# Kernel tuning notes

Hardware: AMD Instinct MI355X
Metric: run time of the kernel (lower is better)

Reference implementation:

```python
import jax, jax.numpy as jnp
import numpy as np

N_CLASSES = 80
TOPK = 13
ALPHA = 1.0
BETA = 6.0
EPS = 1e-9
BS, N_ANCHORS, N_MAX = 32, 8400, 100


def setup_inputs() -> dict:
    key = jax.random.key(0)
    k1, k2, k3, k4, k5, k6 = jax.random.split(key, 6)
    pred_scores = jax.random.uniform(k1, (BS, N_ANCHORS, N_CLASSES), dtype=jnp.float32)
    anchor_points = jax.random.uniform(k2, (N_ANCHORS, 2), dtype=jnp.float32) * 640.0
    # predicted boxes centered on anchor points (valid xyxy)
    wh = jax.random.uniform(k3, (BS, N_ANCHORS, 2), dtype=jnp.float32) * 100.0 + 4.0
    ctr = anchor_points[None]
    pred_bboxes = jnp.concatenate([ctr - wh / 2, ctr + wh / 2], axis=-1)
    gt_lt = jax.random.uniform(k4, (BS, N_MAX, 2), dtype=jnp.float32) * 500.0
    gt_wh = jax.random.uniform(k5, (BS, N_MAX, 2), dtype=jnp.float32) * 120.0 + 8.0
    gt_bboxes = jnp.concatenate([gt_lt, gt_lt + gt_wh], axis=-1)
    gt_labels = jax.random.randint(k6, (BS, N_MAX, 1), 0, N_CLASSES).astype(jnp.int32)
    mask_gt = jnp.ones((BS, N_MAX, 1), dtype=jnp.float32)
    return {"pred_scores": pred_scores, "pred_bboxes": pred_bboxes,
            "anchor_points": anchor_points, "gt_labels": gt_labels,
            "gt_bboxes": gt_bboxes, "mask_gt": mask_gt}


def _batch_iou(a, b):
    # a: [bs, n, 4], b: [bs, m, 4] (xyxy) -> [bs, n, m]
    lt = jnp.maximum(a[:, :, None, :2], b[:, None, :, :2])
    rb = jnp.minimum(a[:, :, None, 2:], b[:, None, :, 2:])
    wh = jnp.clip(rb - lt, 0.0)
    inter = wh[..., 0] * wh[..., 1]
    area_a = ((a[..., 2] - a[..., 0]) * (a[..., 3] - a[..., 1]))[:, :, None]
    area_b = ((b[..., 2] - b[..., 0]) * (b[..., 3] - b[..., 1]))[:, None, :]
    return inter / (area_a + area_b - inter + EPS)


def _assign(pred_scores, pred_bboxes, anchor_points, gt_labels, gt_bboxes, mask_gt):
    bs, n_anchors, n_classes = pred_scores.shape
    n_max = gt_bboxes.shape[1]
    labels = gt_labels[..., 0].astype(jnp.int32)  # [bs, n_max]

    # alignment metric: bbox_scores[b,g,a] = pred_scores[b,a,labels[b,g]]
    ps_t = jnp.swapaxes(pred_scores, 1, 2)  # [bs, C, n_anchors]
    bbox_scores = jnp.take_along_axis(ps_t, labels[:, :, None], axis=1)  # [bs, n_max, n_anchors]
    overlaps = _batch_iou(gt_bboxes, pred_bboxes)  # [bs, n_max, n_anchors]
    align_metric = jnp.power(bbox_scores, ALPHA) * jnp.power(overlaps, BETA)

    # anchor centers inside gt boxes
    ap = anchor_points[None, None, :, :]  # [1,1,n_anchors,2]
    deltas = jnp.concatenate(
        [ap - gt_bboxes[:, :, None, :2], gt_bboxes[:, :, None, 2:] - ap], axis=-1)
    is_in_gts = (deltas.min(axis=-1) > EPS).astype(align_metric.dtype)  # [bs,n_max,n_anchors]

    # topk candidate selection
    metrics = align_metric * is_in_gts
    _, topk_idxs = jax.lax.top_k(metrics, TOPK)  # [bs, n_max, TOPK]
    topk_mask = (mask_gt > 0)  # [bs, n_max, 1], broadcasts over TOPK
    topk_idxs = jnp.where(topk_mask, topk_idxs, 0)

    def count_row(idx):  # idx: [TOPK] -> anchor hit counts [n_anchors]
        return jnp.zeros((n_anchors,), jnp.int32).at[idx].add(1)
    counts = jax.vmap(jax.vmap(count_row))(topk_idxs)  # [bs, n_max, n_anchors]
    is_in_topk = jnp.where(counts > 1, 0, counts).astype(metrics.dtype)

    mask_pos = is_in_topk * is_in_gts * mask_gt  # [bs, n_max, n_anchors]

    # fix collisions: anchors assigned to multiple GTs keep the max-IoU GT
    mask_pos_sum = mask_pos.sum(axis=1)  # [bs, n_anchors]
    multi = mask_pos_sum[:, None, :] > 1
    is_max_overlaps = jax.nn.one_hot(overlaps.argmax(axis=1), n_max, axis=1,
                                     dtype=mask_pos.dtype)  # [bs, n_max, n_anchors]
    mask_pos = jnp.where(multi, is_max_overlaps, mask_pos)
    mask_pos_sum = mask_pos.sum(axis=1)
    assigned_gt_idx = mask_pos.argmax(axis=1)  # [bs, n_anchors]

    # final assignments via flattened gather
    flat_idx = assigned_gt_idx + jnp.arange(bs, dtype=jnp.int32)[:, None] * n_max
    assigned_labels = labels.reshape(-1)[flat_idx]  # [bs, n_anchors]
    assigned_bboxes = gt_bboxes.reshape(-1, 4)[flat_idx]  # [bs, n_anchors, 4]
    assigned_labels = jnp.where(assigned_labels < 0, 0, assigned_labels)
    assigned_scores = jax.nn.one_hot(assigned_labels, n_classes, dtype=pred_scores.dtype)
    pos = mask_pos_sum > 0
    assigned_scores = jnp.where(pos[..., None], assigned_scores, 0.0)
    assigned_labels = jnp.where(pos, assigned_labels, n_classes)

    # normalize scores by alignment metric
    align_metric = align_metric * mask_pos
    pos_align = align_metric.max(axis=-1, keepdims=True)  # [bs, n_max, 1]
    pos_overlaps = (overlaps * mask_pos).max(axis=-1, keepdims=True)
    norm = (align_metric * pos_overlaps / (pos_align + EPS)).max(axis=1)[..., None]  # [bs,n_anchors,1]
    assigned_scores = assigned_scores * norm

    return assigned_labels, assigned_bboxes, assigned_scores, pos


def reference(pred_scores, pred_bboxes, anchor_points, gt_labels, gt_bboxes, mask_gt):
    return _assign(pred_scores, pred_bboxes, anchor_points, gt_labels, gt_bboxes, mask_gt)
```

## Files before the change

kernel.cpp:

```cpp
#include <hip/hip_runtime.h>

#define BS 32
#define NA 8400
#define NMAX 100
#define NC 80
#define TOPK 13
#define EPSF 1e-9f
#define WCAP 1024
#define NSTRIP 64
#define STRIP_INV 0.1f

#define OFF_LBL  0
#define OFF_BOX  (BS*NA)
#define OFF_SCR  (BS*NA + BS*NA*4)
#define OFF_POS  (BS*NA + BS*NA*4 + BS*NA*NC)

#define NBA_ELEMS (BS*NA)
#define ZERO_U32  (NBA_ELEMS + 2*BS*NMAX)

__device__ __forceinline__ float iou_fn(float gx1, float gy1, float gx2, float gy2,
                                        float px1, float py1, float px2, float py2) {
    float lx = fmaxf(gx1, px1), ly = fmaxf(gy1, py1);
    float rx = fminf(gx2, px2), ry = fminf(gy2, py2);
    float w = fmaxf(rx - lx, 0.f), h = fmaxf(ry - ly, 0.f);
    float inter = w * h;
    float aa = (gx2 - gx1) * (gy2 - gy1);
    float ab = (px2 - px1) * (py2 - py1);
    return inter / (aa + ab - inter + EPSF);
}

__global__ __launch_bounds__(1024) void bin_zero_kernel(
    const float* __restrict__ anchor_points,
    int* __restrict__ strip_off, float4* __restrict__ sAPI,
    unsigned int* __restrict__ zero_base)
{
    int t = threadIdx.x;
    if (blockIdx.x != 0) {
        uint4* z = (uint4*)zero_base;
        const int nz = ZERO_U32 / 4;
        uint4 zz = make_uint4(0u, 0u, 0u, 0u);
        for (int i = (blockIdx.x - 1) * 1024 + t; i < nz; i += 8 * 1024)
            z[i] = zz;
        return;
    }

    __shared__ int cnt[NSTRIP];
    __shared__ int cur[NSTRIP];
    if (t < NSTRIP) cnt[t] = 0;
    __syncthreads();
    const float2* ap2 = (const float2*)anchor_points;
    for (int a = t; a < NA; a += 1024) {
        int s = (int)(ap2[a].y * STRIP_INV);
        s = s < 0 ? 0 : (s > NSTRIP - 1 ? NSTRIP - 1 : s);
        atomicAdd(&cnt[s], 1);
    }
    __syncthreads();
    if (t < 64) {
        int v = cnt[t];
        int inc = v;
        #pragma unroll
        for (int d = 1; d < 64; d <<= 1) {
            int o = __shfl_up(inc, d, 64);
            if (t >= d) inc += o;
        }
        int excl = inc - v;
        cur[t] = excl; strip_off[t] = excl;
        if (t == 63) strip_off[64] = inc;
    }
    __syncthreads();
    for (int a = t; a < NA; a += 1024) {
        float2 p = ap2[a];
        int s = (int)(p.y * STRIP_INV);
        s = s < 0 ? 0 : (s > NSTRIP - 1 ? NSTRIP - 1 : s);
        int pos = atomicAdd(&cur[s], 1);
        sAPI[pos] = make_float4(p.x, p.y, __int_as_float(a), 0.f);
    }
}

__global__ __launch_bounds__(256) void topk_kernel(
    const float* __restrict__ pred_scores,
    const float* __restrict__ pred_bboxes,
    const int*   __restrict__ gt_labels,
    const float* __restrict__ gt_bboxes,
    const float* __restrict__ mask_gt,
    const int*   __restrict__ strip_off,
    const float4* __restrict__ sAPI,
    unsigned int* __restrict__ claims)
{
    __shared__ unsigned short aidx[4][WCAP];
    int wave = threadIdx.x >> 6;
    int lane = threadIdx.x & 63;
    int row = blockIdx.x * 4 + wave;
    int b = row / NMAX, j = row % NMAX;
    if (mask_gt[row] <= 0.f) return;

    const float* gbp = gt_bboxes + (size_t)row * 4;
    float gx1 = gbp[0], gy1 = gbp[1], gx2 = gbp[2], gy2 = gbp[3];
    int lab = gt_labels[row];

    int s_lo = (int)(gy1 * STRIP_INV); s_lo = s_lo < 0 ? 0 : (s_lo > NSTRIP-1 ? NSTRIP-1 : s_lo);
    int s_hi = (int)(gy2 * STRIP_INV); s_hi = s_hi < 0 ? 0 : (s_hi > NSTRIP-1 ? NSTRIP-1 : s_hi);
    int lo = strip_off[s_lo], hi = strip_off[s_hi + 1];

    int cnt = 0;
    for (int base = lo; base < hi; base += 64) {
        int p = base + lane;
        bool hit = false; int a = 0;
        if (p < hi) {
            float4 ap = sAPI[p];
            a = __float_as_int(ap.z);
            hit = (ap.x - gx1 > EPSF) && (ap.y - gy1 > EPSF) &&
                  (gx2 - ap.x > EPSF) && (gy2 - ap.y > EPSF);
        }
        unsigned long long mb = __ballot(hit);
        if (hit) {
            int my = cnt + __popcll(mb & ((1ULL << lane) - 1ULL));
            if (my < WCAP) aidx[wave][my] = (unsigned short)a;
        }
        cnt += __popcll(mb);
    }
    if (cnt > WCAP) cnt = WCAP;

    unsigned long long loc[TOPK];
    #pragma unroll
    for (int i = 0; i < TOPK; i++) loc[i] = 0ULL;
    const float4* pb4 = (const float4*)pred_bboxes;
    for (int p = lane; p < cnt; p += 64) {
        int a = aidx[wave][p];
        float4 pb = pb4[b * NA + a];
        float s = pred_scores[((size_t)b * NA + a) * NC + lab];
        float iou = iou_fn(gx1, gy1, gx2, gy2, pb.x, pb.y, pb.z, pb.w);
        float i2 = iou * iou;
        float m = s * (i2 * i2 * i2);
        if (m > 0.f) {
            unsigned long long key =
                ((unsigned long long)__float_as_uint(m) << 32) |
                (unsigned int)(NA - a);
            #pragma unroll
            for (int i = 0; i < TOPK; i++) {
                if (key > loc[i]) { unsigned long long tmp = loc[i]; loc[i] = key; key = tmp; }
            }
        }
    }

    for (int r = 0; r < TOPK; r++) {
        unsigned long long h = loc[0];
        unsigned long long m = h;
        #pragma unroll
        for (int s = 32; s > 0; s >>= 1) {
            unsigned long long o = __shfl_xor(m, s, 64);
            m = o > m ? o : m;
        }
        if (m == 0ULL) break;
        unsigned long long ball = __ballot(h == m);
        if (lane == (int)__builtin_ctzll(ball)) {
            #pragma unroll
            for (int i = 0; i < TOPK - 1; i++) loc[i] = loc[i + 1];
            loc[TOPK - 1] = 0ULL;
            int a = NA - (int)(unsigned int)(m & 0xFFFFFFFFULL);
            atomicAdd(&claims[b * NA + a], (1u << 16) | (unsigned int)j);
        }
    }
}

__global__ __launch_bounds__(256) void resolve_kernel(
    const float* __restrict__ pred_scores,
    const float* __restrict__ pred_bboxes,
    const int*   __restrict__ gt_labels,
    const float* __restrict__ gt_bboxes,
    const unsigned int* __restrict__ claims,
    int* __restrict__ assigned_j, float* __restrict__ a_align,
    unsigned int* __restrict__ pa_bits, unsigned int* __restrict__ po_bits)
{
    __shared__ float4 gtb[NMAX];
    __shared__ int    glab[NMAX];
    int b = blockIdx.y;
    int t = threadIdx.x;
    if (t < NMAX) {
        gtb[t]  = ((const float4*)gt_bboxes)[b * NMAX + t];
        glab[t] = gt_labels[b * NMAX + t];
    }
    __syncthreads();

    int ai = blockIdx.x * 256 + t;
    if (ai >= NA) return;
    int idx = b * NA + ai;
    unsigned int pk = claims[idx];
    if (pk == 0u) { assigned_j[idx] = -1; a_align[idx] = 0.f; return; }

    float4 pb = ((const float4*)pred_bboxes)[idx];

    int js; float iou;
    if ((pk >> 16) == 1u) {
        js = (int)(pk & 0xFFFFu);
        float4 g = gtb[js];
        iou = iou_fn(g.x, g.y, g.z, g.w, pb.x, pb.y, pb.z, pb.w);
    } else {
        float best = -1.f; js = 0;
        for (int j = 0; j < NMAX; j++) {
            float4 g = gtb[j];
            float v = iou_fn(g.x, g.y, g.z, g.w, pb.x, pb.y, pb.z, pb.w);
            if (v > best) { best = v; js = j; }
        }
        iou = best;
    }
    int lab = glab[js];
    float s = pred_scores[(size_t)idx * NC + lab];
    float i2 = iou * iou;
    float align = s * (i2 * i2 * i2);
    assigned_j[idx] = js; a_align[idx] = align;
    atomicMax(&pa_bits[b * NMAX + js], __float_as_uint(align));
    atomicMax(&po_bits[b * NMAX + js], __float_as_uint(iou));
}

__global__ __launch_bounds__(256) void finalize_kernel(
    const int*   __restrict__ gt_labels,
    const float* __restrict__ gt_bboxes,
    const int* __restrict__ assigned_j,
    const float* __restrict__ a_align,
    const unsigned int* __restrict__ pa_bits, const unsigned int* __restrict__ po_bits,
    float* __restrict__ out)
{
    int t = threadIdx.x;
    int idx = blockIdx.x * 256 + t;
    int b = idx / NA;
    int js = assigned_j[idx];
    bool pos = js >= 0;
    int j0 = pos ? js : 0;
    int lab = gt_labels[b * NMAX + j0];

    out[OFF_LBL + idx] = pos ? (float)lab : (float)NC;

    float4 gb = ((const float4*)gt_bboxes)[b * NMAX + j0];
    ((float4*)(out + OFF_BOX))[idx] = gb;

    out[OFF_POS + idx] = pos ? 1.f : 0.f;

    float4* sc = (float4*)(out + OFF_SCR + (size_t)blockIdx.x * 256 * NC);
    float4 z = make_float4(0.f, 0.f, 0.f, 0.f);
    #pragma unroll
    for (int i = 0; i < 256 * NC / 4 / 256; i++)
        sc[t + i * 256] = z;
    __syncthreads();

    if (pos) {
        float pa = __uint_as_float(pa_bits[b * NMAX + js]);
        float po = __uint_as_float(po_bits[b * NMAX + js]);
        float norm = a_align[idx] * po / (pa + EPSF);
        out[OFF_SCR + (size_t)idx * NC + lab] = norm;
    }
}

extern "C" void kernel_launch(void* const* d_in, const int* in_sizes, int n_in,
                              void* d_out, int out_size, void* d_ws, size_t ws_size,
                              hipStream_t stream) {
    const float* pred_scores   = (const float*)d_in[0];
    const float* pred_bboxes   = (const float*)d_in[1];
    const float* anchor_points = (const float*)d_in[2];
    const int*   gt_labels     = (const int*)d_in[3];
    const float* gt_bboxes     = (const float*)d_in[4];
    const float* mask_gt       = (const float*)d_in[5];

    char* ws = (char*)d_ws;
    const size_t NBA = (size_t)BS * NA;
    unsigned int* claims   = (unsigned int*)(ws);
    unsigned int* pa_bits  = (unsigned int*)(ws + NBA * 4);
    unsigned int* po_bits  = (unsigned int*)(ws + NBA * 4 + (size_t)BS * NMAX * 4);
    int*   assigned_j = (int*)(ws + NBA * 4 + (size_t)BS * NMAX * 8);
    float* a_align    = (float*)(ws + NBA * 8 + (size_t)BS * NMAX * 8);
    size_t off5 = NBA * 12 + (size_t)BS * NMAX * 8;
    int*    strip_off = (int*)(ws + off5);
    float4* sAPI      = (float4*)(ws + off5 + 512);

    float* out = (float*)d_out;

    bin_zero_kernel<<<9, 1024, 0, stream>>>(anchor_points, strip_off, sAPI, claims);

    topk_kernel<<<BS * NMAX / 4, 256, 0, stream>>>(
        pred_scores, pred_bboxes, gt_labels, gt_bboxes, mask_gt,
        strip_off, sAPI, claims);

    dim3 rgrid((NA + 255) / 256, BS);
    resolve_kernel<<<rgrid, 256, 0, stream>>>(
        pred_scores, pred_bboxes, gt_labels, gt_bboxes, claims,
        assigned_j, a_align, pa_bits, po_bits);

    finalize_kernel<<<(int)(NBA / 256), 256, 0, stream>>>(
        gt_labels, gt_bboxes, assigned_j, a_align, pa_bits, po_bits, out);
}
```

Before: 231.7 us.

## Drop binning kernel, emit per-GT top-k lists, move score zeroing into topk launch

Removes the anchor strip-binning kernel and has each top-k wave scan all anchors directly. Instead of global atomic claims per anchor, each GT row writes its top-k anchor list and count, and the resolve kernel rebuilds per-anchor claims in shared memory from those lists. Zeroing of the large score output and the pa/po buffers moves into extra blocks of the top-k launch, so it can overlap with the top-k work, and is removed from finalize. This cuts one launch and the global claims buffer traffic. In exchange, every wave scans all 8400 anchors instead of a y-strip, and each resolve block rescans all 1300 list entries.

```diff
diff --git a/kernel.cpp b/kernel.cpp
--- a/kernel.cpp
+++ b/kernel.cpp
@@ -7,16 +7,16 @@
 #define TOPK 13
 #define EPSF 1e-9f
 #define WCAP 1024
-#define NSTRIP 64
-#define STRIP_INV 0.1f
 
 #define OFF_LBL  0
 #define OFF_BOX  (BS*NA)
 #define OFF_SCR  (BS*NA + BS*NA*4)
 #define OFF_POS  (BS*NA + BS*NA*4 + BS*NA*NC)
 
-#define NBA_ELEMS (BS*NA)
-#define ZERO_U32  (NBA_ELEMS + 2*BS*NMAX)
+#define NROWS (BS*NMAX)
+#define TKBLK 800
+#define ZBLK  250
+#define NSC4  (BS*NA*NC/4)
 
 __device__ __forceinline__ float iou_fn(float gx1, float gy1, float gx2, float gy2,
                                         float px1, float py1, float px2, float py2) {
@@ -29,93 +29,61 @@
     return inter / (aa + ab - inter + EPSF);
 }
 
-__global__ __launch_bounds__(1024) void bin_zero_kernel(
-    const float* __restrict__ anchor_points,
-    int* __restrict__ strip_off, float4* __restrict__ sAPI,
-    unsigned int* __restrict__ zero_base)
-{
-    int t = threadIdx.x;
-    if (blockIdx.x != 0) {
-        uint4* z = (uint4*)zero_base;
-        const int nz = ZERO_U32 / 4;
-        uint4 zz = make_uint4(0u, 0u, 0u, 0u);
-        for (int i = (blockIdx.x - 1) * 1024 + t; i < nz; i += 8 * 1024)
-            z[i] = zz;
-        return;
-    }
-
-    __shared__ int cnt[NSTRIP];
-    __shared__ int cur[NSTRIP];
-    if (t < NSTRIP) cnt[t] = 0;
-    __syncthreads();
-    const float2* ap2 = (const float2*)anchor_points;
-    for (int a = t; a < NA; a += 1024) {
-        int s = (int)(ap2[a].y * STRIP_INV);
-        s = s < 0 ? 0 : (s > NSTRIP - 1 ? NSTRIP - 1 : s);
-        atomicAdd(&cnt[s], 1);
-    }
-    __syncthreads();
-    if (t < 64) {
-        int v = cnt[t];
-        int inc = v;
-        #pragma unroll
-        for (int d = 1; d < 64; d <<= 1) {
-            int o = __shfl_up(inc, d, 64);
-            if (t >= d) inc += o;
-        }
-        int excl = inc - v;
-        cur[t] = excl; strip_off[t] = excl;
-        if (t == 63) strip_off[64] = inc;
-    }
-    __syncthreads();
-    for (int a = t; a < NA; a += 1024) {
-        float2 p = ap2[a];
-        int s = (int)(p.y * STRIP_INV);
-        s = s < 0 ? 0 : (s > NSTRIP - 1 ? NSTRIP - 1 : s);
-        int pos = atomicAdd(&cur[s], 1);
-        sAPI[pos] = make_float4(p.x, p.y, __int_as_float(a), 0.f);
-    }
-}
-
 __global__ __launch_bounds__(256) void topk_kernel(
     const float* __restrict__ pred_scores,
     const float* __restrict__ pred_bboxes,
+    const float* __restrict__ anchor_points,
     const int*   __restrict__ gt_labels,
     const float* __restrict__ gt_bboxes,
     const float* __restrict__ mask_gt,
-    const int*   __restrict__ strip_off,
-    const float4* __restrict__ sAPI,
-    unsigned int* __restrict__ claims)
+    unsigned int*   __restrict__ ccount,
+    unsigned short* __restrict__ clist,
+    unsigned int* __restrict__ pa_bits,
+    unsigned int* __restrict__ po_bits,
+    float* __restrict__ out)
 {
+    int t = threadIdx.x;
+    if (blockIdx.x >= TKBLK) {
+        int zb = blockIdx.x - TKBLK;
+        if (zb == 0) {
+            uint4* pz = (uint4*)pa_bits;
+            uint4 zz = make_uint4(0u, 0u, 0u, 0u);
+            for (int i = t; i < 1600; i += 256) pz[i] = zz;
+        }
+        float4* sz = (float4*)(out + OFF_SCR);
+        float4 zf = make_float4(0.f, 0.f, 0.f, 0.f);
+        for (int i = zb * 256 + t; i < NSC4; i += ZBLK * 256) sz[i] = zf;
+        return;
+    }
+
     __shared__ unsigned short aidx[4][WCAP];
-    int wave = threadIdx.x >> 6;
-    int lane = threadIdx.x & 63;
+    int wave = t >> 6;
+    int lane = t & 63;
     int row = blockIdx.x * 4 + wave;
-    int b = row / NMAX, j = row % NMAX;
-    if (mask_gt[row] <= 0.f) return;
+    if (mask_gt[row] <= 0.f) {
+        if (lane == 0) ccount[row] = 0u;
+        return;
+    }
+    int b = row / NMAX;
 
     const float* gbp = gt_bboxes + (size_t)row * 4;
     float gx1 = gbp[0], gy1 = gbp[1], gx2 = gbp[2], gy2 = gbp[3];
     int lab = gt_labels[row];
 
-    int s_lo = (int)(gy1 * STRIP_INV); s_lo = s_lo < 0 ? 0 : (s_lo > NSTRIP-1 ? NSTRIP-1 : s_lo);
-    int s_hi = (int)(gy2 * STRIP_INV); s_hi = s_hi < 0 ? 0 : (s_hi > NSTRIP-1 ? NSTRIP-1 : s_hi);
-    int lo = strip_off[s_lo], hi = strip_off[s_hi + 1];
-
+    const float2* ap2 = (const float2*)anchor_points;
     int cnt = 0;
-    for (int base = lo; base < hi; base += 64) {
+    for (int base = 0; base < NA; base += 64) {
         int p = base + lane;
-        bool hit = false; int a = 0;
-        if (p < hi) {
-            float4 ap = sAPI[p];
-            a = __float_as_int(ap.z);
+        bool hit = false;
+        if (p < NA) {
+            float2 ap = ap2[p];
             hit = (ap.x - gx1 > EPSF) && (ap.y - gy1 > EPSF) &&
                   (gx2 - ap.x > EPSF) && (gy2 - ap.y > EPSF);
         }
         unsigned long long mb = __ballot(hit);
         if (hit) {
             int my = cnt + __popcll(mb & ((1ULL << lane) - 1ULL));
-            if (my < WCAP) aidx[wave][my] = (unsigned short)a;
+            if (my < WCAP) aidx[wave][my] = (unsigned short)p;
         }
         cnt += __popcll(mb);
     }
@@ -143,6 +111,7 @@
         }
     }
 
+    int picks = TOPK;
     for (int r = 0; r < TOPK; r++) {
         unsigned long long h = loc[0];
         unsigned long long m = h;
@@ -151,16 +120,17 @@
             unsigned long long o = __shfl_xor(m, s, 64);
             m = o > m ? o : m;
         }
-        if (m == 0ULL) break;
+        if (m == 0ULL) { picks = r; break; }
         unsigned long long ball = __ballot(h == m);
         if (lane == (int)__builtin_ctzll(ball)) {
             #pragma unroll
             for (int i = 0; i < TOPK - 1; i++) loc[i] = loc[i + 1];
             loc[TOPK - 1] = 0ULL;
             int a = NA - (int)(unsigned int)(m & 0xFFFFFFFFULL);
-            atomicAdd(&claims[b * NA + a], (1u << 16) | (unsigned int)j);
-        }
-    }
+            clist[row * TOPK + r] = (unsigned short)a;
+        }
+    }
+    if (lane == 0) ccount[row] = (unsigned int)picks;
 }
 
 __global__ __launch_bounds__(256) void resolve_kernel(
@@ -168,28 +138,43 @@
     const float* __restrict__ pred_bboxes,
     const int*   __restrict__ gt_labels,
     const float* __restrict__ gt_bboxes,
-    const unsigned int* __restrict__ claims,
+    const unsigned int*   __restrict__ ccount,
+    const unsigned short* __restrict__ clist,
     int* __restrict__ assigned_j, float* __restrict__ a_align,
     unsigned int* __restrict__ pa_bits, unsigned int* __restrict__ po_bits)
 {
     __shared__ float4 gtb[NMAX];
     __shared__ int    glab[NMAX];
+    __shared__ int    ccnt[NMAX];
+    __shared__ unsigned int pkl[256];
     int b = blockIdx.y;
     int t = threadIdx.x;
     if (t < NMAX) {
         gtb[t]  = ((const float4*)gt_bboxes)[b * NMAX + t];
         glab[t] = gt_labels[b * NMAX + t];
-    }
+        ccnt[t] = (int)ccount[b * NMAX + t];
+    }
+    pkl[t] = 0u;
     __syncthreads();
 
-    int ai = blockIdx.x * 256 + t;
+    int lo = blockIdx.x * 256;
+    for (int e = t; e < NMAX * TOPK; e += 256) {
+        int j = e / TOPK, k = e - j * TOPK;
+        if (k < ccnt[j]) {
+            int a = clist[(b * NMAX + j) * TOPK + k];
+            unsigned int w = (unsigned int)(a - lo);
+            if (w < 256u) atomicAdd(&pkl[w], (1u << 16) | (unsigned int)j);
+        }
+    }
+    __syncthreads();
+
+    int ai = lo + t;
     if (ai >= NA) return;
     int idx = b * NA + ai;
-    unsigned int pk = claims[idx];
+    unsigned int pk = pkl[t];
     if (pk == 0u) { assigned_j[idx] = -1; a_align[idx] = 0.f; return; }
 
     float4 pb = ((const float4*)pred_bboxes)[idx];
-
     int js; float iou;
     if ((pk >> 16) == 1u) {
         js = (int)(pk & 0xFFFFu);
@@ -230,24 +215,13 @@
     int lab = gt_labels[b * NMAX + j0];
 
     out[OFF_LBL + idx] = pos ? (float)lab : (float)NC;
-
-    float4 gb = ((const float4*)gt_bboxes)[b * NMAX + j0];
-    ((float4*)(out + OFF_BOX))[idx] = gb;
-
+    ((float4*)(out + OFF_BOX))[idx] = ((const float4*)gt_bboxes)[b * NMAX + j0];
     out[OFF_POS + idx] = pos ? 1.f : 0.f;
-
-    float4* sc = (float4*)(out + OFF_SCR + (size_t)blockIdx.x * 256 * NC);
-    float4 z = make_float4(0.f, 0.f, 0.f, 0.f);
-    #pragma unroll
-    for (int i = 0; i < 256 * NC / 4 / 256; i++)
-        sc[t + i * 256] = z;
-    __syncthreads();
 
     if (pos) {
         float pa = __uint_as_float(pa_bits[b * NMAX + js]);
         float po = __uint_as_float(po_bits[b * NMAX + js]);
-        float norm = a_align[idx] * po / (pa + EPSF);
-        out[OFF_SCR + (size_t)idx * NC + lab] = norm;
+        out[OFF_SCR + (size_t)idx * NC + lab] = a_align[idx] * po / (pa + EPSF);
     }
 }
 
@@ -263,26 +237,22 @@
 
     char* ws = (char*)d_ws;
     const size_t NBA = (size_t)BS * NA;
-    unsigned int* claims   = (unsigned int*)(ws);
-    unsigned int* pa_bits  = (unsigned int*)(ws + NBA * 4);
-    unsigned int* po_bits  = (unsigned int*)(ws + NBA * 4 + (size_t)BS * NMAX * 4);
-    int*   assigned_j = (int*)(ws + NBA * 4 + (size_t)BS * NMAX * 8);
-    float* a_align    = (float*)(ws + NBA * 8 + (size_t)BS * NMAX * 8);
-    size_t off5 = NBA * 12 + (size_t)BS * NMAX * 8;
-    int*    strip_off = (int*)(ws + off5);
-    float4* sAPI      = (float4*)(ws + off5 + 512);
+    unsigned int*   pa_bits = (unsigned int*)(ws);
+    unsigned int*   po_bits = (unsigned int*)(ws + 12800);
+    unsigned int*   ccount  = (unsigned int*)(ws + 25600);
+    unsigned short* clist   = (unsigned short*)(ws + 38400);
+    int*   assigned_j = (int*)(ws + 38400 + (size_t)NROWS * TOPK * 2 + 320);
+    float* a_align    = (float*)((char*)assigned_j + NBA * 4);
 
     float* out = (float*)d_out;
 
-    bin_zero_kernel<<<9, 1024, 0, stream>>>(anchor_points, strip_off, sAPI, claims);
-
-    topk_kernel<<<BS * NMAX / 4, 256, 0, stream>>>(
-        pred_scores, pred_bboxes, gt_labels, gt_bboxes, mask_gt,
-        strip_off, sAPI, claims);
+    topk_kernel<<<TKBLK + ZBLK, 256, 0, stream>>>(
+        pred_scores, pred_bboxes, anchor_points, gt_labels, gt_bboxes, mask_gt,
+        ccount, clist, pa_bits, po_bits, out);
 
     dim3 rgrid((NA + 255) / 256, BS);
     resolve_kernel<<<rgrid, 256, 0, stream>>>(
-        pred_scores, pred_bboxes, gt_labels, gt_bboxes, claims,
+        pred_scores, pred_bboxes, gt_labels, gt_bboxes, ccount, clist,
         assigned_j, a_align, pa_bits, po_bits);
 
     finalize_kernel<<<(int)(NBA / 256), 256, 0, stream>>>(
```

Result: slower. 268.8 us (+16.0%).
